# Optimization experiments

Measured on AMD Instinct MI355X. Metric: run time of the kernel, lower is better.

Reference implementation:

```python
import jax, jax.numpy as jnp
import numpy as np

N_NODES = 20000
N_EDGES = 160000
F_IN = 128
H1 = 1024  # 128 * out_channels
H2 = 512   # 64 * out_channels
OUT = 8    # out_channels


def graph_conv(x, src, dst, w_rel, b_rel, w_root):
    # PyG GraphConv(aggr='mean'): out = lin_rel(mean_{j->i} x_j) + lin_root(x_i)
    n = x.shape[0]
    agg = jax.ops.segment_sum(x[src], dst, num_segments=n)          # [N, F_in]
    deg = jax.ops.segment_sum(jnp.ones((src.shape[0],), x.dtype), dst, num_segments=n)
    mean = agg / jnp.maximum(deg, 1.0)[:, None]
    return mean @ w_rel + b_rel + x @ w_root


def setup_inputs() -> dict:
    key = jax.random.key(0)
    ks = jax.random.split(key, 12)
    x = jax.random.normal(ks[0], (N_NODES, F_IN), dtype=jnp.float32)
    edge_index = jax.random.randint(ks[1], (2, N_EDGES), 0, N_NODES, dtype=jnp.int64)

    def lin(k, fi, fo):
        return jax.random.normal(k, (fi, fo), dtype=jnp.float32) / np.sqrt(fi)

    return {
        "x": x,
        "edge_index": edge_index,
        "w1_rel": lin(ks[2], F_IN, H1), "b1": jnp.zeros((H1,), jnp.float32), "w1_root": lin(ks[3], F_IN, H1),
        "w2_rel": lin(ks[4], H1, H2), "b2": jnp.zeros((H2,), jnp.float32), "w2_root": lin(ks[5], H1, H2),
        "wmu_rel": lin(ks[6], H2, OUT), "bmu": jnp.zeros((OUT,), jnp.float32), "wmu_root": lin(ks[7], H2, OUT),
        "wls_rel": lin(ks[8], H2, OUT), "bls": jnp.zeros((OUT,), jnp.float32), "wls_root": lin(ks[9], H2, OUT),
    }


def reference(x, edge_index, w1_rel, b1, w1_root, w2_rel, b2, w2_root,
              wmu_rel, bmu, wmu_root, wls_rel, bls, wls_root):
    src, dst = edge_index[0], edge_index[1]
    h = jax.nn.relu(graph_conv(x, src, dst, w1_rel, b1, w1_root))
    h = jax.nn.relu(graph_conv(h, src, dst, w2_rel, b2, w2_root))
    mu = graph_conv(h, src, dst, wmu_rel, bmu, wmu_root)
    logstd = graph_conv(h, src, dst, wls_rel, bls, wls_root)
    return (mu, logstd)
```

## Files before the change

kernel.cpp:

```cpp
#include <hip/hip_runtime.h>

typedef __attribute__((ext_vector_type(8))) short short8;
typedef __attribute__((ext_vector_type(4))) float f32x4;
typedef unsigned long long u64;

__device__ __forceinline__ unsigned short f2bf(float f) {
  union { float f; unsigned u; } v; v.f = f;
  unsigned u = v.u;
  unsigned r = (u + 0x7FFFu + ((u >> 16) & 1u)) >> 16;
  return (unsigned short)r;
}
__device__ __forceinline__ float bf2f(unsigned short s) {
  union { unsigned u; float f; } v; v.u = ((unsigned)s) << 16;
  return v.f;
}

__device__ __forceinline__ void gl_lds16(const unsigned short* g, unsigned short* l) {
  __builtin_amdgcn_global_load_lds(
      (const __attribute__((address_space(1))) void*)g,
      (__attribute__((address_space(3))) void*)l, 16, 0, 0);
}


__device__ __forceinline__ void ttile(const float* __restrict__ src, int Nw,
                                      unsigned short* __restrict__ dst, int ldd,
                                      int rowoff, int coloff,
                                      int tileIdx, int tilesN, float (*tile)[33]) {
  int tk = tileIdx / tilesN, tn = tileIdx % tilesN;
  int k0 = tk * 32, n0 = tn * 32;
  int tx = threadIdx.x & 31, ty = threadIdx.x >> 5;
#pragma unroll
  for (int s = 0; s < 4; ++s)
    tile[ty + s * 8][tx] = src[(size_t)(k0 + ty + s * 8) * Nw + n0 + tx];
  __syncthreads();
#pragma unroll
  for (int s = 0; s < 4; ++s)
    dst[(size_t)(rowoff + n0 + ty + s * 8) * ldd + coloff + k0 + tx] =
        f2bf(tile[tx][ty + s * 8]);
}

__global__ void prep_kernel(int* deg, int* cursor, int n, int* flag,
                            const float* __restrict__ w1_rel, const float* __restrict__ w1_root,
                            const float* __restrict__ w2_rel, const float* __restrict__ w2_root,
                            const float* __restrict__ wmu_rel, const float* __restrict__ wmu_root,
                            const float* __restrict__ wls_rel, const float* __restrict__ wls_root,
                            unsigned short* __restrict__ Bt1,
                            unsigned short* __restrict__ Bt2,
                            unsigned short* __restrict__ Bt3) {
  __shared__ float tile[32][33];
  int b = blockIdx.x;
  if (b >= 1344) {
    int i = (b - 1344) * blockDim.x + threadIdx.x;
    int stride = 64 * blockDim.x;
    for (int j = i; j < n; j += stride) { deg[j] = 0; cursor[j] = 0; }
    if (i == 0) *flag = 1;
    return;
  }
  if (b < 128)       ttile(w1_rel, 1024, Bt1, 256, 0, 0, b, 32, tile);
  else if (b < 256)  ttile(w1_root, 1024, Bt1, 256, 0, 128, b - 128, 32, tile);
  else if (b < 768)  ttile(w2_rel, 512, Bt2, 1024, 0, 0, b - 256, 16, tile);
  else if (b < 1280) ttile(w2_root, 512, Bt2, 1024, 512, 0, b - 768, 16, tile);
  else {
    int idx = (b - 1280) * 256 + threadIdx.x;
    int nn = idx >> 9, k = idx & 511;
    float v;
    if (nn < 8) v = wmu_rel[(size_t)k * 8 + nn];
    else if (nn < 16) v = wmu_root[(size_t)k * 8 + (nn - 8)];
    else if (nn < 24) v = wls_rel[(size_t)k * 8 + (nn - 16)];
    else v = wls_root[(size_t)k * 8 + (nn - 24)];
    Bt3[(size_t)nn * 512 + k] = f2bf(v);
  }
}

__global__ void detect_kernel(const long long* p, int nslots, int n_nodes, int* flag) {
  int i = blockIdx.x * blockDim.x + threadIdx.x;
  if (i < nslots) {
    long long v = p[i];
    if (v < 0 || v >= n_nodes) atomicAnd(flag, 0);
  }
}

__device__ __forceinline__ int edge_at(const void* p, int is64, size_t idx) {
  return is64 ? (int)((const long long*)p)[idx] : ((const int*)p)[idx];
}

__global__ void count_kernel(const void* edges, int E, const int* flag, int* deg) {
  int is64 = *flag;
  int i = blockIdx.x * blockDim.x + threadIdx.x;
  int stride = gridDim.x * blockDim.x;
  for (int e = i; e < E; e += stride) {
    int d = edge_at(edges, is64, (size_t)E + e);
    atomicAdd(&deg[d], 1);
  }
}

__global__ void scan_kernel(const int* __restrict__ deg, int* __restrict__ rs,
                            float* __restrict__ invdeg, int n) {
  __shared__ int ssum[1024];
  int tid = threadIdx.x;
  int chunk = (n + 1023) >> 10;
  int start = tid * chunk;
  int end = min(start + chunk, n);
  int s = 0;
  for (int i = start; i < end; ++i) s += deg[i];
  ssum[tid] = s;
  __syncthreads();
  for (int off = 1; off < 1024; off <<= 1) {
    int t = (tid >= off) ? ssum[tid - off] : 0;
    __syncthreads();
    ssum[tid] += t;
    __syncthreads();
  }
  int run = (tid ? ssum[tid - 1] : 0);
  if (tid == 0) rs[0] = 0;
  for (int i = start; i < end; ++i) {
    int d = deg[i];
    run += d;
    rs[i + 1] = run;
    invdeg[i] = 1.0f / fmaxf((float)d, 1.0f);
  }
}

__global__ void fill_kernel(const void* edges, int E, const int* flag,
                            const int* __restrict__ rs, int* cursor, int* col_src) {
  int is64 = *flag;
  int i = blockIdx.x * blockDim.x + threadIdx.x;
  int stride = gridDim.x * blockDim.x;
  for (int e = i; e < E; e += stride) {
    int d = edge_at(edges, is64, (size_t)E + e);
    int s = edge_at(edges, is64, (size_t)e);
    int p = atomicAdd(&cursor[d], 1);
    col_src[rs[d] + p] = s;
  }
}


__global__ void agg1_kernel(const float* __restrict__ x,
                            const int* __restrict__ rs, const int* __restrict__ cs,
                            const float* __restrict__ invdeg,
                            unsigned short* __restrict__ A1) {
  int node = blockIdx.x;
  int f = threadIdx.x;
  float xi = x[(size_t)node * 128 + f];
  float acc = 0.f;
  int e1 = rs[node + 1];
  for (int e = rs[node]; e < e1; ++e) {
    acc += x[(size_t)cs[e] * 128 + f];
  }
  A1[(size_t)node * 256 + f] = f2bf(acc * invdeg[node]);
  A1[(size_t)node * 256 + 128 + f] = f2bf(xi);
}

__global__ void agg2_kernel(const unsigned short* __restrict__ P2,
                            const int* __restrict__ rs, const int* __restrict__ cs,
                            const float* __restrict__ invdeg,
                            const float* __restrict__ b2,
                            unsigned short* __restrict__ h2, int M) {
  int node = blockIdx.x * 2 + (threadIdx.x >> 6);
  if (node >= M) return;
  int f0 = (threadIdx.x & 63) * 8;
  float acc[8];
#pragma unroll
  for (int v = 0; v < 8; ++v) acc[v] = 0.f;
  int e1 = rs[node + 1];
  for (int e = rs[node]; e < e1; ++e) {
    int s = cs[e];
    uint4 w = *reinterpret_cast<const uint4*>(P2 + (size_t)s * 1024 + f0);
    acc[0] += bf2f((unsigned short)(w.x & 0xffff));
    acc[1] += bf2f((unsigned short)(w.x >> 16));
    acc[2] += bf2f((unsigned short)(w.y & 0xffff));
    acc[3] += bf2f((unsigned short)(w.y >> 16));
    acc[4] += bf2f((unsigned short)(w.z & 0xffff));
    acc[5] += bf2f((unsigned short)(w.z >> 16));
    acc[6] += bf2f((unsigned short)(w.w & 0xffff));
    acc[7] += bf2f((unsigned short)(w.w >> 16));
  }
  float inv = invdeg[node];
  uint4 wr = *reinterpret_cast<const uint4*>(P2 + (size_t)node * 1024 + 512 + f0);
  float rt[8] = {
    bf2f((unsigned short)(wr.x & 0xffff)), bf2f((unsigned short)(wr.x >> 16)),
    bf2f((unsigned short)(wr.y & 0xffff)), bf2f((unsigned short)(wr.y >> 16)),
    bf2f((unsigned short)(wr.z & 0xffff)), bf2f((unsigned short)(wr.z >> 16)),
    bf2f((unsigned short)(wr.w & 0xffff)), bf2f((unsigned short)(wr.w >> 16))};
  unsigned short o[8];
#pragma unroll
  for (int v = 0; v < 8; ++v)
    o[v] = f2bf(fmaxf(acc[v] * inv + rt[v] + b2[f0 + v], 0.f));
  uint4 pk;
  pk.x = (unsigned)o[0] | ((unsigned)o[1] << 16);
  pk.y = (unsigned)o[2] | ((unsigned)o[3] << 16);
  pk.z = (unsigned)o[4] | ((unsigned)o[5] << 16);
  pk.w = (unsigned)o[6] | ((unsigned)o[7] << 16);
  *reinterpret_cast<uint4*>(h2 + (size_t)node * 512 + f0) = pk;
}

__global__ void head_agg_kernel(const float* __restrict__ P3,
                                const int* __restrict__ rs, const int* __restrict__ cs,
                                const float* __restrict__ invdeg,
                                const float* __restrict__ bmu, const float* __restrict__ bls,
                                float* __restrict__ outmu, float* __restrict__ outls, int M) {
  int idx = blockIdx.x * blockDim.x + threadIdx.x;
  int node = idx >> 4;
  int c = idx & 15;
  if (node >= M) return;
  int relc = (c < 8) ? c : (16 + (c - 8));
  float acc = 0.f;
  int e1 = rs[node + 1];
  for (int e = rs[node]; e < e1; ++e) acc += P3[(size_t)cs[e] * 32 + relc];
  float v = acc * invdeg[node] + P3[(size_t)node * 32 + relc + 8]
          + ((c < 8) ? bmu[c] : bls[c - 8]);
  if (c < 8) outmu[(size_t)node * 8 + c] = v;
  else outls[(size_t)node * 8 + (c - 8)] = v;
}

__launch_bounds__(256, 4)
__global__ void gemm_db_kernel(const unsigned short* __restrict__ A, int lda,
                               const unsigned short* __restrict__ Bt, int ldb,
                               const float* __restrict__ bias,
                               void* __restrict__ outp, int ldo,
                               int M, int N, int K, int relu, int out_f32, int gx) {
  __shared__ unsigned short As[2 * 4096];
  __shared__ unsigned short Bs[2 * 4096];
  const int tid = threadIdx.x;
  const int lane = tid & 63;
  const int w = tid >> 6;
  const int wr = w >> 1, wc = w & 1;
  const int lr = lane & 15, lk = lane >> 4;
  const int sw8 = (lk ^ ((lr >> 1) & 3)) * 8;

  int nwg = gridDim.x, orig = blockIdx.x;
  int q = nwg >> 3, r = nwg & 7;
  int xcd = orig & 7, lid = orig >> 3;
  int swz = (xcd < r ? xcd * (q + 1) : r * (q + 1) + (xcd - r) * q) + lid;
  int m0 = (swz / gx) * 128, n0 = (swz % gx) * 128;

  f32x4 acc[4][4];
#pragma unroll
  for (int i = 0; i < 4; ++i)
#pragma unroll
    for (int j = 0; j < 4; ++j) acc[i][j] = (f32x4)0.0f;

  const int r0 = tid >> 2;
  const int slog = ((tid & 3) ^ ((r0 >> 1) & 3)) * 8;
  const unsigned short* gA = A + (size_t)(m0 + r0) * lda + slog;
  const unsigned short* gB = Bt + (size_t)(n0 + r0) * ldb + slog;
  const size_t a64 = (size_t)64 * lda, b64 = (size_t)64 * ldb;
  unsigned short* wa = As + w * 512;
  unsigned short* wb = Bs + w * 512;

  auto STG = [&](int s, int t) {
    const unsigned short* a = gA + (size_t)t * 32;
    const unsigned short* b = gB + (size_t)t * 32;
    gl_lds16(a, wa + s * 4096);
    gl_lds16(a + a64, wa + s * 4096 + 2048);
    gl_lds16(b, wb + s * 4096);
    gl_lds16(b + b64, wb + s * 4096 + 2048);
  };

  const int nt = K >> 5;
  STG(0, 0);
  asm volatile("s_waitcnt vmcnt(0)" ::: "memory");
  __builtin_amdgcn_s_barrier();

  int buf = 0;
  for (int t = 0; t < nt; ++t) {
    if (t + 1 < nt) STG(buf ^ 1, t + 1);
    const unsigned short* as_ = As + buf * 4096;
    const unsigned short* bs_ = Bs + buf * 4096;
    short8 af[4], bf[4];
#pragma unroll
    for (int i = 0; i < 4; ++i) {
      af[i] = *reinterpret_cast<const short8*>(&as_[(wr * 64 + i * 16 + lr) * 32 + sw8]);
      bf[i] = *reinterpret_cast<const short8*>(&bs_[(wc * 64 + i * 16 + lr) * 32 + sw8]);
    }
    __builtin_amdgcn_s_setprio(1);
#pragma unroll
    for (int i = 0; i < 4; ++i)
#pragma unroll
      for (int j = 0; j < 4; ++j)
        acc[i][j] = __builtin_amdgcn_mfma_f32_16x16x32_bf16(af[i], bf[j], acc[i][j], 0, 0, 0);
    __builtin_amdgcn_s_setprio(0);
    if (t + 1 < nt) {
      asm volatile("s_waitcnt vmcnt(0) lgkmcnt(0)" ::: "memory");
      __builtin_amdgcn_s_barrier();
    }
    buf ^= 1;
  }

#pragma unroll
  for (int i = 0; i < 4; ++i) {
    int row_b = m0 + wr * 64 + i * 16 + lk * 4;
#pragma unroll
    for (int j = 0; j < 4; ++j) {
      int col = n0 + wc * 64 + j * 16 + lr;
      float bv = bias ? bias[col] : 0.f;
#pragma unroll
      for (int rr = 0; rr < 4; ++rr) {
        int row = row_b + rr;
        if (row < M) {
          float v = acc[i][j][rr] + bv;
          if (relu) v = fmaxf(v, 0.f);
          if (out_f32) ((float*)outp)[(size_t)row * ldo + col] = v;
          else ((unsigned short*)outp)[(size_t)row * ldo + col] = f2bf(v);
        }
      }
    }
  }
}

__launch_bounds__(256, 3)
__global__ void gemm_heads_kernel(const unsigned short* __restrict__ A,
                                  const unsigned short* __restrict__ Bt3,
                                  float* __restrict__ P3, int M, int gx_unused) {
  __shared__ unsigned short Bs[16 * 1024];
  __shared__ unsigned short As[2 * 4096];
  const int tid = threadIdx.x;
  const int lane = tid & 63;
  const int w = tid >> 6;
  const int lr = lane & 15, lk = lane >> 4;
  const int sw8 = (lk ^ ((lr >> 1) & 3)) * 8;

  int nwg = gridDim.x, orig = blockIdx.x;
  int q = nwg >> 3, r = nwg & 7;
  int xcd = orig & 7, lid = orig >> 3;
  int swz = (xcd < r ? xcd * (q + 1) : r * (q + 1) + (xcd - r) * q) + lid;
  int m0 = swz * 128;

  for (int i = 0; i < 8; ++i) {
    int j = i * 256 + tid;
    int n = j >> 6, p = j & 63;
    int x = (n >> 1) & 3;
    uint4 v = *reinterpret_cast<const uint4*>(Bt3 + (size_t)n * 512 + ((p & ~3) | ((p & 3) ^ x)) * 8);
    *reinterpret_cast<uint4*>(&Bs[(p >> 2) * 1024 + n * 32 + (p & 3) * 8]) = v;
  }

  f32x4 acc[2][2];
#pragma unroll
  for (int i = 0; i < 2; ++i)
#pragma unroll
    for (int j = 0; j < 2; ++j) acc[i][j] = (f32x4)0.0f;

  const int r0 = tid >> 2;
  const int slog = ((tid & 3) ^ ((r0 >> 1) & 3)) * 8;
  const unsigned short* gA = A + (size_t)(m0 + r0) * 512 + slog;
  const size_t a64 = (size_t)64 * 512;
  unsigned short* wa = As + w * 512;

  auto STG = [&](int s, int t) {
    const unsigned short* a = gA + (size_t)t * 32;
    gl_lds16(a, wa + s * 4096);
    gl_lds16(a + a64, wa + s * 4096 + 2048);
  };

  STG(0, 0);
  __syncthreads();

  int buf = 0;
  const int nt = 16;
  for (int t = 0; t < nt; ++t) {
    if (t + 1 < nt) STG(buf ^ 1, t + 1);
    const unsigned short* as_ = As + buf * 4096;
    short8 af[2], bf[2];
#pragma unroll
    for (int i = 0; i < 2; ++i) {
      af[i] = *reinterpret_cast<const short8*>(&as_[(w * 32 + i * 16 + lr) * 32 + sw8]);
      bf[i] = *reinterpret_cast<const short8*>(&Bs[t * 1024 + (i * 16 + lr) * 32 + sw8]);
    }
#pragma unroll
    for (int i = 0; i < 2; ++i)
#pragma unroll
      for (int j = 0; j < 2; ++j)
        acc[i][j] = __builtin_amdgcn_mfma_f32_16x16x32_bf16(af[i], bf[j], acc[i][j], 0, 0, 0);
    if (t + 1 < nt) {
      asm volatile("s_waitcnt vmcnt(0) lgkmcnt(0)" ::: "memory");
      __builtin_amdgcn_s_barrier();
    }
    buf ^= 1;
  }

#pragma unroll
  for (int i = 0; i < 2; ++i) {
    int row_b = m0 + w * 32 + i * 16 + lk * 4;
#pragma unroll
    for (int j = 0; j < 2; ++j) {
      int col = j * 16 + lr;
#pragma unroll
      for (int rr = 0; rr < 4; ++rr) {
        int row = row_b + rr;
        if (row < M) P3[(size_t)row * 32 + col] = acc[i][j][rr];
      }
    }
  }
}


extern "C" void kernel_launch(void* const* d_in, const int* in_sizes, int n_in,
                              void* d_out, int out_size, void* d_ws, size_t ws_size,
                              hipStream_t stream) {
  const float* x = (const float*)d_in[0];
  const void* edge = d_in[1];
  const float* w1_rel = (const float*)d_in[2];
  const float* b1 = (const float*)d_in[3];
  const float* w1_root = (const float*)d_in[4];
  const float* w2_rel = (const float*)d_in[5];
  const float* b2 = (const float*)d_in[6];
  const float* w2_root = (const float*)d_in[7];
  const float* wmu_rel = (const float*)d_in[8];
  const float* bmu = (const float*)d_in[9];
  const float* wmu_root = (const float*)d_in[10];
  const float* wls_rel = (const float*)d_in[11];
  const float* bls = (const float*)d_in[12];
  const float* wls_root = (const float*)d_in[13];

  const int FIN = 128, H1 = 1024, H2 = 512;
  const int M = in_sizes[0] / FIN;
  const int E = in_sizes[1] / 2;
  const int Mpad = ((M + 127) / 128) * 128;
  const int gy = Mpad / 128;

  char* ws = (char*)d_ws;
  size_t off = 0;
  auto alloc = [&](size_t bytes) -> char* {
    char* p = ws + off;
    off = (off + bytes + 255) & ~(size_t)255;
    return p;
  };
  int* flag = (int*)alloc(4);
  int* deg = (int*)alloc((size_t)M * 4);
  int* cursor = (int*)alloc((size_t)M * 4);
  int* rs = (int*)alloc((size_t)(M + 1) * 4);
  float* invdeg = (float*)alloc((size_t)M * 4);
  int* cs = (int*)alloc((size_t)E * 4);
  unsigned short* A1 = (unsigned short*)alloc((size_t)Mpad * 256 * 2);
  unsigned short* h1 = (unsigned short*)alloc((size_t)Mpad * 1024 * 2);
  unsigned short* P2 = (unsigned short*)alloc((size_t)Mpad * 1024 * 2);
  unsigned short* h2 = (unsigned short*)alloc((size_t)Mpad * 512 * 2);
  float* P3 = (float*)alloc((size_t)Mpad * 32 * 4);
  unsigned short* Bt1 = (unsigned short*)alloc((size_t)H1 * 256 * 2);
  unsigned short* Bt2 = (unsigned short*)alloc((size_t)1024 * 1024 * 2);
  unsigned short* Bt3 = (unsigned short*)alloc((size_t)32 * 512 * 2);

  prep_kernel<<<1408, 256, 0, stream>>>(deg, cursor, M, flag,
                                        w1_rel, w1_root, w2_rel, w2_root,
                                        wmu_rel, wmu_root, wls_rel, wls_root,
                                        Bt1, Bt2, Bt3);
  detect_kernel<<<8, 256, 0, stream>>>((const long long*)edge, 2048, M, flag);
  count_kernel<<<256, 256, 0, stream>>>(edge, E, flag, deg);
  scan_kernel<<<1, 1024, 0, stream>>>(deg, rs, invdeg, M);
  fill_kernel<<<256, 256, 0, stream>>>(edge, E, flag, rs, cursor, cs);

  agg1_kernel<<<M, 128, 0, stream>>>(x, rs, cs, invdeg, A1);
  gemm_db_kernel<<<(H1 / 128) * gy, 256, 0, stream>>>(
      A1, 256, Bt1, 256, b1, h1, 1024, M, H1, 256, 1, 0, H1 / 128);

  gemm_db_kernel<<<(1024 / 128) * gy, 256, 0, stream>>>(
      h1, 1024, Bt2, 1024, nullptr, P2, 1024, M, 1024, 1024, 0, 0, 1024 / 128);
  agg2_kernel<<<(M + 1) / 2, 128, 0, stream>>>(P2, rs, cs, invdeg, b2, h2, M);

  gemm_heads_kernel<<<gy, 256, 0, stream>>>(h2, Bt3, P3, M, 1);
  float* outmu = (float*)d_out;
  float* outls = outmu + (size_t)M * 8;
  head_agg_kernel<<<(M * 16 + 255) / 256, 256, 0, stream>>>(
      P3, rs, cs, invdeg, bmu, bls, outmu, outls, M);
}
```

Baseline: 269.6 us.

## Store GEMM operands in tile-packed layout and process two tiles per block

Weight matrices, the layer-1 input A1 and the layer-1 output h1 are now written in a 128x32 tile-packed layout, so each K-step tile load in the GEMM reads one contiguous 8 KB chunk instead of strided rows. The GEMM kernel also loops over two output tiles per workgroup and launches half as many blocks. This aims to improve load coalescing and cut per-block launch overhead. The cost is scattered writes in the producers and reduced parallelism, plus an extra barrier between tiles. It depends on gy being even and on every consumer of h1 expecting the packed layout.

```diff
diff --git a/kernel.cpp b/kernel.cpp
--- a/kernel.cpp
+++ b/kernel.cpp
@@ -15,6 +15,11 @@
   return v.f;
 }
 
+__device__ __forceinline__ size_t pkaddr(int row, int col, int K) {
+  return ((size_t)(row >> 7) * (K >> 5) + (col >> 5)) * 4096 +
+         ((row & 127) << 5) + (col & 31);
+}
+
 __device__ __forceinline__ void gl_lds16(const unsigned short* g, unsigned short* l) {
   __builtin_amdgcn_global_load_lds(
       (const __attribute__((address_space(1))) void*)g,
@@ -23,7 +28,7 @@
 
 
 __device__ __forceinline__ void ttile(const float* __restrict__ src, int Nw,
-                                      unsigned short* __restrict__ dst, int ldd,
+                                      unsigned short* __restrict__ dst, int Kd,
                                       int rowoff, int coloff,
                                       int tileIdx, int tilesN, float (*tile)[33]) {
   int tk = tileIdx / tilesN, tn = tileIdx % tilesN;
@@ -35,7 +40,7 @@
   __syncthreads();
 #pragma unroll
   for (int s = 0; s < 4; ++s)
-    dst[(size_t)(rowoff + n0 + ty + s * 8) * ldd + coloff + k0 + tx] =
+    dst[pkaddr(rowoff + n0 + ty + s * 8, coloff + k0 + tx, Kd)] =
         f2bf(tile[tx][ty + s * 8]);
 }
 
@@ -147,8 +152,8 @@
   for (int e = rs[node]; e < e1; ++e) {
     acc += x[(size_t)cs[e] * 128 + f];
   }
-  A1[(size_t)node * 256 + f] = f2bf(acc * invdeg[node]);
-  A1[(size_t)node * 256 + 128 + f] = f2bf(xi);
+  A1[pkaddr(node, f, 256)] = f2bf(acc * invdeg[node]);
+  A1[pkaddr(node, 128 + f, 256)] = f2bf(xi);
 }
 
 __global__ void agg2_kernel(const unsigned short* __restrict__ P2,
@@ -214,11 +219,11 @@
 }
 
 __launch_bounds__(256, 4)
-__global__ void gemm_db_kernel(const unsigned short* __restrict__ A, int lda,
-                               const unsigned short* __restrict__ Bt, int ldb,
+__global__ void gemm_db_kernel(const unsigned short* __restrict__ A,
+                               const unsigned short* __restrict__ Bt,
                                const float* __restrict__ bias,
                                void* __restrict__ outp, int ldo,
-                               int M, int N, int K, int relu, int out_f32, int gx) {
+                               int M, int K, int relu, int out_f32, int out_pk, int gx) {
   __shared__ unsigned short As[2 * 4096];
   __shared__ unsigned short Bs[2 * 4096];
   const int tid = threadIdx.x;
@@ -232,76 +237,82 @@
   int q = nwg >> 3, r = nwg & 7;
   int xcd = orig & 7, lid = orig >> 3;
   int swz = (xcd < r ? xcd * (q + 1) : r * (q + 1) + (xcd - r) * q) + lid;
-  int m0 = (swz / gx) * 128, n0 = (swz % gx) * 128;
-
-  f32x4 acc[4][4];
-#pragma unroll
-  for (int i = 0; i < 4; ++i)
-#pragma unroll
-    for (int j = 0; j < 4; ++j) acc[i][j] = (f32x4)0.0f;
 
   const int r0 = tid >> 2;
   const int slog = ((tid & 3) ^ ((r0 >> 1) & 3)) * 8;
-  const unsigned short* gA = A + (size_t)(m0 + r0) * lda + slog;
-  const unsigned short* gB = Bt + (size_t)(n0 + r0) * ldb + slog;
-  const size_t a64 = (size_t)64 * lda, b64 = (size_t)64 * ldb;
+  const int thr_off = r0 * 32 + slog;
+  const int nt = K >> 5;
   unsigned short* wa = As + w * 512;
   unsigned short* wb = Bs + w * 512;
 
-  auto STG = [&](int s, int t) {
-    const unsigned short* a = gA + (size_t)t * 32;
-    const unsigned short* b = gB + (size_t)t * 32;
-    gl_lds16(a, wa + s * 4096);
-    gl_lds16(a + a64, wa + s * 4096 + 2048);
-    gl_lds16(b, wb + s * 4096);
-    gl_lds16(b + b64, wb + s * 4096 + 2048);
-  };
-
-  const int nt = K >> 5;
-  STG(0, 0);
-  asm volatile("s_waitcnt vmcnt(0)" ::: "memory");
-  __builtin_amdgcn_s_barrier();
-
-  int buf = 0;
-  for (int t = 0; t < nt; ++t) {
-    if (t + 1 < nt) STG(buf ^ 1, t + 1);
-    const unsigned short* as_ = As + buf * 4096;
-    const unsigned short* bs_ = Bs + buf * 4096;
-    short8 af[4], bf[4];
+  for (int tt = 0; tt < 2; ++tt) {
+    int tileIdx = swz * 2 + tt;
+    int m0 = (tileIdx / gx) * 128, n0 = (tileIdx % gx) * 128;
+    const unsigned short* gA = A + (size_t)(m0 >> 7) * nt * 4096 + thr_off;
+    const unsigned short* gB = Bt + (size_t)(n0 >> 7) * nt * 4096 + thr_off;
+
+    f32x4 acc[4][4];
+#pragma unroll
+    for (int i = 0; i < 4; ++i)
+#pragma unroll
+      for (int j = 0; j < 4; ++j) acc[i][j] = (f32x4)0.0f;
+
+    auto STG = [&](int s, int t) {
+      const unsigned short* a = gA + (size_t)t * 4096;
+      const unsigned short* b = gB + (size_t)t * 4096;
+      gl_lds16(a, wa + s * 4096);
+      gl_lds16(a + 2048, wa + s * 4096 + 2048);
+      gl_lds16(b, wb + s * 4096);
+      gl_lds16(b + 2048, wb + s * 4096 + 2048);
+    };
+
+    if (tt) __builtin_amdgcn_s_barrier();
+    STG(0, 0);
+    asm volatile("s_waitcnt vmcnt(0)" ::: "memory");
+    __builtin_amdgcn_s_barrier();
+
+    int buf = 0;
+    for (int t = 0; t < nt; ++t) {
+      if (t + 1 < nt) STG(buf ^ 1, t + 1);
+      const unsigned short* as_ = As + buf * 4096;
+      const unsigned short* bs_ = Bs + buf * 4096;
+      short8 af[4], bf[4];
+#pragma unroll
+      for (int i = 0; i < 4; ++i) {
+        af[i] = *reinterpret_cast<const short8*>(&as_[(wr * 64 + i * 16 + lr) * 32 + sw8]);
+        bf[i] = *reinterpret_cast<const short8*>(&bs_[(wc * 64 + i * 16 + lr) * 32 + sw8]);
+      }
+      __builtin_amdgcn_s_setprio(1);
+#pragma unroll
+      for (int i = 0; i < 4; ++i)
+#pragma unroll
+        for (int j = 0; j < 4; ++j)
+          acc[i][j] = __builtin_amdgcn_mfma_f32_16x16x32_bf16(af[i], bf[j], acc[i][j], 0, 0, 0);
+      __builtin_amdgcn_s_setprio(0);
+      if (t + 1 < nt) {
+        asm volatile("s_waitcnt vmcnt(0) lgkmcnt(0)" ::: "memory");
+        __builtin_amdgcn_s_barrier();
+      }
+      buf ^= 1;
+    }
+
 #pragma unroll
     for (int i = 0; i < 4; ++i) {
-      af[i] = *reinterpret_cast<const short8*>(&as_[(wr * 64 + i * 16 + lr) * 32 + sw8]);
-      bf[i] = *reinterpret_cast<const short8*>(&bs_[(wc * 64 + i * 16 + lr) * 32 + sw8]);
-    }
-    __builtin_amdgcn_s_setprio(1);
-#pragma unroll
-    for (int i = 0; i < 4; ++i)
-#pragma unroll
-      for (int j = 0; j < 4; ++j)
-        acc[i][j] = __builtin_amdgcn_mfma_f32_16x16x32_bf16(af[i], bf[j], acc[i][j], 0, 0, 0);
-    __builtin_amdgcn_s_setprio(0);
-    if (t + 1 < nt) {
-      asm volatile("s_waitcnt vmcnt(0) lgkmcnt(0)" ::: "memory");
-      __builtin_amdgcn_s_barrier();
-    }
-    buf ^= 1;
-  }
-
-#pragma unroll
-  for (int i = 0; i < 4; ++i) {
-    int row_b = m0 + wr * 64 + i * 16 + lk * 4;
-#pragma unroll
-    for (int j = 0; j < 4; ++j) {
-      int col = n0 + wc * 64 + j * 16 + lr;
-      float bv = bias ? bias[col] : 0.f;
-#pragma unroll
-      for (int rr = 0; rr < 4; ++rr) {
-        int row = row_b + rr;
-        if (row < M) {
-          float v = acc[i][j][rr] + bv;
-          if (relu) v = fmaxf(v, 0.f);
-          if (out_f32) ((float*)outp)[(size_t)row * ldo + col] = v;
-          else ((unsigned short*)outp)[(size_t)row * ldo + col] = f2bf(v);
+      int row_b = m0 + wr * 64 + i * 16 + lk * 4;
+#pragma unroll
+      for (int j = 0; j < 4; ++j) {
+        int col = n0 + wc * 64 + j * 16 + lr;
+        float bv = bias ? bias[col] : 0.f;
+#pragma unroll
+        for (int rr = 0; rr < 4; ++rr) {
+          int row = row_b + rr;
+          if (row < M) {
+            float v = acc[i][j][rr] + bv;
+            if (relu) v = fmaxf(v, 0.f);
+            if (out_f32) ((float*)outp)[(size_t)row * ldo + col] = v;
+            else if (out_pk) ((unsigned short*)outp)[pkaddr(row, col, ldo)] = f2bf(v);
+            else ((unsigned short*)outp)[(size_t)row * ldo + col] = f2bf(v);
+          }
         }
       }
     }
@@ -450,11 +461,11 @@
   fill_kernel<<<256, 256, 0, stream>>>(edge, E, flag, rs, cursor, cs);
 
   agg1_kernel<<<M, 128, 0, stream>>>(x, rs, cs, invdeg, A1);
-  gemm_db_kernel<<<(H1 / 128) * gy, 256, 0, stream>>>(
-      A1, 256, Bt1, 256, b1, h1, 1024, M, H1, 256, 1, 0, H1 / 128);
-
-  gemm_db_kernel<<<(1024 / 128) * gy, 256, 0, stream>>>(
-      h1, 1024, Bt2, 1024, nullptr, P2, 1024, M, 1024, 1024, 0, 0, 1024 / 128);
+  gemm_db_kernel<<<(H1 / 128) * gy / 2, 256, 0, stream>>>(
+      A1, Bt1, b1, h1, 1024, M, 256, 1, 0, 1, H1 / 128);
+
+  gemm_db_kernel<<<(1024 / 128) * gy / 2, 256, 0, stream>>>(
+      h1, Bt2, nullptr, P2, 1024, M, 1024, 0, 0, 0, 1024 / 128);
   agg2_kernel<<<(M + 1) / 2, 128, 0, stream>>>(P2, rs, cs, invdeg, b2, h2, M);
 
   gemm_heads_kernel<<<gy, 256, 0, stream>>>(h2, Bt3, P3, M, 1);
```

Result: no change. 271.2 us (+0.6%).
